# Performance work log

Measured on AMD Instinct MI355X. Metric: run time of the kernel, lower is better.

## Reference

```python
import jax, jax.numpy as jnp
import numpy as np

C = 256
NH = 4  # attention heads
G = 8   # groupnorm groups
EPS = 1e-5


def group_norm(x, weight, bias):
    B, Cc, H, W = x.shape
    xg = x.reshape(B, G, Cc // G, H, W)
    mean = xg.mean(axis=(2, 3, 4), keepdims=True)
    var = xg.var(axis=(2, 3, 4), keepdims=True)
    xg = (xg - mean) * jax.lax.rsqrt(var + EPS)
    xn = xg.reshape(B, Cc, H, W)
    return xn * weight[None, :, None, None] + bias[None, :, None, None]


def setup_inputs() -> dict:
    key = jax.random.key(0)
    ks = jax.random.split(key, 7)
    B, H, W = 16, 32, 32
    x = jax.random.normal(ks[0], (B, C, H, W), dtype=jnp.float32)
    n_weight = jnp.ones((C,), dtype=jnp.float32)
    n_bias = jnp.zeros((C,), dtype=jnp.float32)
    qkv_w = jax.random.normal(ks[1], (3 * C, C), dtype=jnp.float32) * (C ** -0.5)
    qkv_b = jnp.zeros((3 * C,), dtype=jnp.float32)
    p_w = jax.random.normal(ks[2], (C, C), dtype=jnp.float32) * (C ** -0.5)
    p_b = jnp.zeros((C,), dtype=jnp.float32)
    return {"x": x, "n_weight": n_weight, "n_bias": n_bias,
            "qkv_w": qkv_w, "qkv_b": qkv_b, "p_w": p_w, "p_b": p_b}


def reference(x, n_weight, n_bias, qkv_w, qkv_b, p_w, p_b):
    B, Cc, H, W = x.shape
    N = H * W
    dh = Cc // NH
    sc = dh ** -0.5
    xn = group_norm(x, n_weight, n_bias)  # [B,C,H,W]
    xn_flat = xn.reshape(B, Cc, N)
    # 1x1 conv == channel matmul
    qkv = jnp.einsum('oc,bcn->bon', qkv_w, xn_flat) + qkv_b[None, :, None]
    qkv = qkv.reshape(B, 3, NH, dh, N)
    q, k, v = qkv[:, 0], qkv[:, 1], qkv[:, 2]  # [B,h,dh,N]
    a = jax.nn.softmax(jnp.einsum('bhci,bhcj->bhij', q, k) * sc, axis=-1)
    o = jnp.einsum('bhij,bhcj->bhci', a, v).reshape(B, Cc, N)
    proj = jnp.einsum('oc,bcn->bon', p_w, o) + p_b[None, :, None]
    return x + proj.reshape(B, Cc, H, W)
```

## Files before the change

kernel.cpp:

```cpp
#include <hip/hip_runtime.h>
#include <math.h>

typedef unsigned short ushort;
typedef unsigned int uint;
typedef __attribute__((ext_vector_type(8))) short bf16x8;
typedef __attribute__((ext_vector_type(4))) float f32x4;

constexpr int Bc  = 16;
constexpr float EPSc = 1e-5f;
constexpr float QSC  = 0.18033688f;

__device__ inline ushort f2bf(float f) {
    uint u = __float_as_uint(f);
    uint r = (u + 0x7fffu + ((u >> 16) & 1u)) >> 16;
    return (ushort)r;
}
__device__ inline uint pack2(float a, float b) {
    return (uint)f2bf(a) | ((uint)f2bf(b) << 16);
}
__device__ __forceinline__ uint cvt2(float a, float b) {
#if __has_builtin(__builtin_amdgcn_cvt_pk_bf16_f32)
    auto v = __builtin_amdgcn_cvt_pk_bf16_f32(a, b);
    uint u; __builtin_memcpy(&u, &v, 4); return u;
#else
    return pack2(a, b);
#endif
}
#if __has_builtin(__builtin_amdgcn_exp2f)
#define EXP2F(x) __builtin_amdgcn_exp2f(x)
#else
#define EXP2F(x) __expf((x) * 0.69314718f)
#endif
__device__ __forceinline__ void gl_lds16(const ushort* g, ushort* l) {
    __builtin_amdgcn_global_load_lds(
        (const __attribute__((address_space(1))) void*)g,
        (__attribute__((address_space(3))) void*)l, 16, 0, 0);
}

__global__ __launch_bounds__(256) void pre_k(
    const float* __restrict__ x, const float* __restrict__ qkvw,
    const float* __restrict__ pw, float* __restrict__ pstats,
    ushort* __restrict__ wqb, ushort* __restrict__ pwb) {
    int blk = blockIdx.x;
    if (blk < 512) {
        int bg = blk >> 2, part = blk & 3;
        const float4* p = (const float4*)(x + (size_t)bg * 32768 + part * 8192);
        float s = 0.f, s2 = 0.f;
        for (int i = threadIdx.x; i < 2048; i += 256) {
            float4 v = p[i];
            s += v.x + v.y + v.z + v.w;
            s2 += v.x*v.x + v.y*v.y + v.z*v.z + v.w*v.w;
        }
        __shared__ float rs[256], rq[256];
        rs[threadIdx.x] = s; rq[threadIdx.x] = s2;
        __syncthreads();
        for (int off = 128; off > 0; off >>= 1) {
            if (threadIdx.x < (unsigned)off) {
                rs[threadIdx.x] += rs[threadIdx.x + off];
                rq[threadIdx.x] += rq[threadIdx.x + off];
            }
            __syncthreads();
        }
        if (threadIdx.x == 0) {
            pstats[blk * 2]     = rs[0];
            pstats[blk * 2 + 1] = rq[0];
        }
    } else {
        int idx = ((blk - 512) * 256 + threadIdx.x) * 4;
        if (idx < 196608) {
            int row = idx >> 8;
            float sc = (row < 256) ? QSC : 1.f;
            float4 v = *(const float4*)&qkvw[idx];
            uint2 u; u.x = pack2(v.x * sc, v.y * sc); u.y = pack2(v.z * sc, v.w * sc);
            *(uint2*)&wqb[idx] = u;
        } else {
            int j = idx - 196608;
            float4 v = *(const float4*)&pw[j];
            uint2 u; u.x = pack2(v.x, v.y); u.y = pack2(v.z, v.w);
            *(uint2*)&pwb[j] = u;
        }
    }
}

__global__ __launch_bounds__(256) void norm_t_k(
    const float* __restrict__ x, const float* __restrict__ pstats,
    const float* __restrict__ nw, const float* __restrict__ nb,
    ushort* __restrict__ xt) {
    int b = blockIdx.z, ct = blockIdx.y, nt = blockIdx.x;
    __shared__ ushort T[64 * 72];
    int t = threadIdx.x;
    int nn4 = (t & 15) * 4;
#pragma unroll
    for (int p = 0; p < 4; ++p) {
        int cl = (t >> 4) + p * 16;
        int c = ct * 64 + cl;
        int g = c >> 5;
        int base = (b * 8 + g) * 8;
        float s  = (pstats[base] + pstats[base+2]) + (pstats[base+4] + pstats[base+6]);
        float s2 = (pstats[base+1] + pstats[base+3]) + (pstats[base+5] + pstats[base+7]);
        float inv_n = 1.f / 32768.f;
        float mean = s * inv_n;
        float var  = s2 * inv_n - mean * mean;
        float inv  = rsqrtf(var + EPSc);
        float sw = inv * nw[c];
        float sb = nb[c] - mean * sw;
        float4 v = *(const float4*)&x[((size_t)(b * 256 + c)) * 1024 + nt * 64 + nn4];
        T[(nn4 + 0) * 72 + cl] = f2bf(v.x * sw + sb);
        T[(nn4 + 1) * 72 + cl] = f2bf(v.y * sw + sb);
        T[(nn4 + 2) * 72 + cl] = f2bf(v.z * sw + sb);
        T[(nn4 + 3) * 72 + cl] = f2bf(v.w * sw + sb);
    }
    __syncthreads();
#pragma unroll
    for (int p = 0; p < 4; ++p) {
        int nn = (t >> 4) + p * 16;
        int c4 = (t & 15) * 4;
        uint2 w = *(const uint2*)&T[nn * 72 + c4];
        *(uint2*)&xt[((size_t)b * 1024 + nt * 64 + nn) * 256 + ct * 64 + c4] = w;
    }
}

__global__ __launch_bounds__(256, 2) void qkv_gemm_k(
    const ushort* __restrict__ wq, const ushort* __restrict__ xt,
    const float* __restrict__ wb, ushort* __restrict__ qkT,
    ushort* __restrict__ vbuf) {
    int b = blockIdx.z, cy = blockIdx.y, sx = blockIdx.x;
    __shared__ ushort SB[2][2][128 * 64];
    int t = threadIdx.x, lane = t & 63, w = t >> 6;
    int quad = lane >> 4, l15 = lane & 15;
    int wm = w >> 1, wn = w & 1;
    const ushort* wrow = wq + (size_t)cy * 128 * 256;
    const ushort* xrow = xt + ((size_t)b * 1024 + sx * 128) * 256;
    bool tpath = (cy < 4);
    int r0 = t >> 3;
    int cs = (t & 7) ^ (r0 & 7);
    int dst = t * 8;
#pragma unroll
    for (int ps = 0; ps < 4; ++ps) {
        int r = r0 + ps * 32;
        gl_lds16(&wrow[(size_t)r * 256 + cs * 8], &SB[0][0][ps * 2048 + dst]);
        gl_lds16(&xrow[(size_t)r * 256 + cs * 8], &SB[0][1][ps * 2048 + dst]);
    }
    __syncthreads();
    int s0 = quad ^ (l15 & 7);
    f32x4 acc[4][4] = {};
    int cur = 0;
    for (int ki = 0; ki < 4; ++ki) {
        if (ki < 3) {
            int k0 = (ki + 1) * 64, nx = cur ^ 1;
#pragma unroll
            for (int ps = 0; ps < 4; ++ps) {
                int r = r0 + ps * 32;
                gl_lds16(&wrow[(size_t)r * 256 + k0 + cs * 8], &SB[nx][0][ps * 2048 + dst]);
                gl_lds16(&xrow[(size_t)r * 256 + k0 + cs * 8], &SB[nx][1][ps * 2048 + dst]);
            }
        }
        const ushort* Wc = SB[cur][0];
        const ushort* Xc = SB[cur][1];
        const ushort* Am = tpath ? Xc : Wc;
        const ushort* Bn = tpath ? Wc : Xc;
#pragma unroll
        for (int kk = 0; kk < 2; ++kk) {
            int sl = s0 ^ (kk * 4);
            bf16x8 fa[4], fb[4];
#pragma unroll
            for (int mi = 0; mi < 4; ++mi)
                fa[mi] = *(const bf16x8*)&Am[(wm * 64 + mi * 16 + l15) * 64 + sl * 8];
#pragma unroll
            for (int ni = 0; ni < 4; ++ni)
                fb[ni] = *(const bf16x8*)&Bn[(wn * 64 + ni * 16 + l15) * 64 + sl * 8];
#pragma unroll
            for (int mi = 0; mi < 4; ++mi)
#pragma unroll
                for (int ni = 0; ni < 4; ++ni)
                    acc[mi][ni] = __builtin_amdgcn_mfma_f32_16x16x32_bf16(
                        fa[mi], fb[ni], acc[mi][ni], 0, 0, 0);
        }
        __syncthreads();
        cur ^= 1;
    }
    ushort* Tw = ((ushort*)SB) + w * (64 * 72);
    float bsc = (tpath && cy < 2) ? QSC : 1.f;
    if (tpath) {
#pragma unroll
        for (int ni = 0; ni < 4; ++ni) {
            float bias = wb[cy * 128 + wn * 64 + ni * 16 + l15] * bsc;
#pragma unroll
            for (int mi = 0; mi < 4; ++mi)
#pragma unroll
                for (int rr = 0; rr < 4; ++rr)
                    Tw[(mi * 16 + quad * 4 + rr) * 72 + ni * 16 + l15] =
                        f2bf(acc[mi][ni][rr] + bias);
        }
    } else {
#pragma unroll
        for (int mi = 0; mi < 4; ++mi)
#pragma unroll
            for (int rr = 0; rr < 4; ++rr) {
                float bias = wb[cy * 128 + wm * 64 + mi * 16 + quad * 4 + rr];
#pragma unroll
                for (int ni = 0; ni < 4; ++ni)
                    Tw[(mi * 16 + quad * 4 + rr) * 72 + ni * 16 + l15] =
                        f2bf(acc[mi][ni][rr] + bias);
            }
    }
    __asm__ __volatile__("" ::: "memory");
    int row8 = lane >> 3, ch = lane & 7;
#pragma unroll
    for (int p = 0; p < 8; ++p) {
        int row = p * 8 + row8;
        uint4 u = *(const uint4*)&Tw[row * 72 + ch * 8];
        if (tpath) {
            int sp = sx * 128 + wm * 64 + row;
            *(uint4*)&qkT[((size_t)b * 1024 + sp) * 512 + cy * 128 + wn * 64 + ch * 8] = u;
        } else {
            int chanloc = (cy - 4) * 128 + wm * 64 + row;
            *(uint4*)&vbuf[((size_t)b * 256 + chanloc) * 1024 + sx * 128 + wn * 64 + ch * 8] = u;
        }
    }
}

__global__ __launch_bounds__(256, 3) void attn_k(
    const ushort* __restrict__ qkT, const ushort* __restrict__ vbuf,
    ushort* __restrict__ ot) {
    int i0 = blockIdx.x * 128;
    int bh = blockIdx.y;
    int b = bh >> 2, h = bh & 3;
    const ushort* qTb = qkT + (size_t)b * 1024 * 512 + h * 64;
    const ushort* kTb = qTb + 256;
    const ushort* vb  = vbuf + ((size_t)(b * 256 + h * 64)) * 1024;
    __shared__ ushort Ks[2][4096], Vs[2][4096];
    __shared__ ushort Ps[8 * 1152];
    __shared__ float  Lx[128];
    int t = threadIdx.x, lane = t & 63, w = t >> 6;
    int quad = lane >> 4, l15 = lane & 15;
    bf16x8 aq[2][2];
#pragma unroll
    for (int rb = 0; rb < 2; ++rb) {
        const ushort* qr = &qTb[(size_t)(i0 + rb * 64 + w * 16 + l15) * 512];
        aq[rb][0] = *(const bf16x8*)&qr[quad * 8];
        aq[rb][1] = *(const bf16x8*)&qr[32 + quad * 8];
    }
    int r0 = t >> 3;
    int cs = (t & 7) ^ (r0 & 7);
    int p0 = quad ^ (l15 & 7);
    int p1 = p0 ^ 4;
    gl_lds16(&kTb[(size_t)r0 * 512 + cs * 8],        &Ks[0][t * 8]);
    gl_lds16(&kTb[(size_t)(r0 + 32) * 512 + cs * 8], &Ks[0][t * 8 + 2048]);
    gl_lds16(&vb[(size_t)r0 * 1024 + cs * 8],        &Vs[0][t * 8]);
    gl_lds16(&vb[(size_t)(r0 + 32) * 1024 + cs * 8], &Vs[0][t * 8 + 2048]);
    __syncthreads();
    float lsum0 = 0.f, lsum1 = 0.f;
    f32x4 oacc[2][4] = {};
    ushort* Pw0 = &Ps[(w * 2 + 0) * 1152];
    ushort* Pw1 = &Ps[(w * 2 + 1) * 1152];
    int cur = 0;
    for (int j0 = 0; j0 < 1024; j0 += 64) {
        if (j0 < 960) {
            int jn = j0 + 64, nx = cur ^ 1;
            gl_lds16(&kTb[(size_t)(jn + r0) * 512 + cs * 8],        &Ks[nx][t * 8]);
            gl_lds16(&kTb[(size_t)(jn + r0 + 32) * 512 + cs * 8],   &Ks[nx][t * 8 + 2048]);
            gl_lds16(&vb[(size_t)r0 * 1024 + jn + cs * 8],          &Vs[nx][t * 8]);
            gl_lds16(&vb[(size_t)(r0 + 32) * 1024 + jn + cs * 8],   &Vs[nx][t * 8 + 2048]);
        }
        const ushort* Kc = Ks[cur];
        const ushort* Vc = Vs[cur];
        f32x4 s0[4], s1[4];
#pragma unroll
        for (int jt = 0; jt < 4; ++jt) {
            int row = jt * 16 + l15;
            bf16x8 bk0 = *(const bf16x8*)&Kc[row * 64 + p0 * 8];
            bf16x8 bk1 = *(const bf16x8*)&Kc[row * 64 + p1 * 8];
            f32x4 a = {0.f, 0.f, 0.f, 0.f};
            a = __builtin_amdgcn_mfma_f32_16x16x32_bf16(bk0, aq[0][0], a, 0, 0, 0);
            a = __builtin_amdgcn_mfma_f32_16x16x32_bf16(bk1, aq[0][1], a, 0, 0, 0);
            s0[jt] = a;
            f32x4 c = {0.f, 0.f, 0.f, 0.f};
            c = __builtin_amdgcn_mfma_f32_16x16x32_bf16(bk0, aq[1][0], c, 0, 0, 0);
            c = __builtin_amdgcn_mfma_f32_16x16x32_bf16(bk1, aq[1][1], c, 0, 0, 0);
            s1[jt] = c;
        }
#pragma unroll
        for (int jt = 0; jt < 4; ++jt) {
            int o = l15 * 72 + jt * 16 + quad * 4;
            float e0 = EXP2F(s0[jt][0]), e1 = EXP2F(s0[jt][1]);
            float e2 = EXP2F(s0[jt][2]), e3 = EXP2F(s0[jt][3]);
            lsum0 += (e0 + e1) + (e2 + e3);
            *(uint*)&Pw0[o]     = cvt2(e0, e1);
            *(uint*)&Pw0[o + 2] = cvt2(e2, e3);
            float f0 = EXP2F(s1[jt][0]), f1 = EXP2F(s1[jt][1]);
            float f2 = EXP2F(s1[jt][2]), f3 = EXP2F(s1[jt][3]);
            lsum1 += (f0 + f1) + (f2 + f3);
            *(uint*)&Pw1[o]     = cvt2(f0, f1);
            *(uint*)&Pw1[o + 2] = cvt2(f2, f3);
        }
        __asm__ __volatile__("" ::: "memory");
        bf16x8 ap00 = *(const bf16x8*)&Pw0[l15 * 72 + quad * 8];
        bf16x8 ap01 = *(const bf16x8*)&Pw0[l15 * 72 + 32 + quad * 8];
        bf16x8 ap10 = *(const bf16x8*)&Pw1[l15 * 72 + quad * 8];
        bf16x8 ap11 = *(const bf16x8*)&Pw1[l15 * 72 + 32 + quad * 8];
#pragma unroll
        for (int ct = 0; ct < 4; ++ct) {
            int row = ct * 16 + l15;
            bf16x8 bv0 = *(const bf16x8*)&Vc[row * 64 + p0 * 8];
            bf16x8 bv1 = *(const bf16x8*)&Vc[row * 64 + p1 * 8];
            oacc[0][ct] = __builtin_amdgcn_mfma_f32_16x16x32_bf16(ap00, bv0, oacc[0][ct], 0, 0, 0);
            oacc[0][ct] = __builtin_amdgcn_mfma_f32_16x16x32_bf16(ap01, bv1, oacc[0][ct], 0, 0, 0);
            oacc[1][ct] = __builtin_amdgcn_mfma_f32_16x16x32_bf16(ap10, bv0, oacc[1][ct], 0, 0, 0);
            oacc[1][ct] = __builtin_amdgcn_mfma_f32_16x16x32_bf16(ap11, bv1, oacc[1][ct], 0, 0, 0);
        }
        __syncthreads();
        cur ^= 1;
    }
    lsum0 += __shfl_xor(lsum0, 16); lsum0 += __shfl_xor(lsum0, 32);
    lsum1 += __shfl_xor(lsum1, 16); lsum1 += __shfl_xor(lsum1, 32);
    if (quad == 0) {
        Lx[w * 16 + l15]      = lsum0;
        Lx[64 + w * 16 + l15] = lsum1;
    }
    __asm__ __volatile__("" ::: "memory");
#pragma unroll
    for (int rb = 0; rb < 2; ++rb) {
        float4 lv = *(const float4*)&Lx[rb * 64 + w * 16 + quad * 4];
        float linv[4] = {1.f / lv.x, 1.f / lv.y, 1.f / lv.z, 1.f / lv.w};
        ushort* Pw = (rb == 0) ? Pw0 : Pw1;
#pragma unroll
        for (int ct = 0; ct < 4; ++ct)
#pragma unroll
            for (int rr = 0; rr < 4; ++rr)
                Pw[(quad * 4 + rr) * 72 + ct * 16 + l15] = f2bf(oacc[rb][ct][rr] * linv[rr]);
        __asm__ __volatile__("" ::: "memory");
#pragma unroll
        for (int p = 0; p < 2; ++p) {
            int row = p * 8 + (lane >> 3), ch = lane & 7;
            uint4 u = *(const uint4*)&Pw[row * 72 + ch * 8];
            *(uint4*)&ot[((size_t)b * 1024 + i0 + rb * 64 + w * 16 + row) * 256 + h * 64 + ch * 8] = u;
        }
    }
}

__global__ __launch_bounds__(256, 2) void proj_k(
    const ushort* __restrict__ pwb, const ushort* __restrict__ ot,
    const float* __restrict__ pb, const float* __restrict__ x,
    float* __restrict__ out) {
    int b = blockIdx.z, cy = blockIdx.y, sx = blockIdx.x;
    __shared__ ushort SB[2][2][128 * 64];
    int t = threadIdx.x, lane = t & 63, w = t >> 6;
    int quad = lane >> 4, l15 = lane & 15;
    int wm = w >> 1, wn = w & 1;
    const ushort* wrow = pwb + (size_t)cy * 128 * 256;
    const ushort* xrow = ot + ((size_t)b * 1024 + sx * 128) * 256;
    int r0 = t >> 3;
    int cs = (t & 7) ^ (r0 & 7);
    int dst = t * 8;
#pragma unroll
    for (int ps = 0; ps < 4; ++ps) {
        int r = r0 + ps * 32;
        gl_lds16(&wrow[(size_t)r * 256 + cs * 8], &SB[0][0][ps * 2048 + dst]);
        gl_lds16(&xrow[(size_t)r * 256 + cs * 8], &SB[0][1][ps * 2048 + dst]);
    }
    __syncthreads();
    int s0 = quad ^ (l15 & 7);
    f32x4 acc[4][4] = {};
    int cur = 0;
    for (int ki = 0; ki < 4; ++ki) {
        if (ki < 3) {
            int k0 = (ki + 1) * 64, nx = cur ^ 1;
#pragma unroll
            for (int ps = 0; ps < 4; ++ps) {
                int r = r0 + ps * 32;
                gl_lds16(&wrow[(size_t)r * 256 + k0 + cs * 8], &SB[nx][0][ps * 2048 + dst]);
                gl_lds16(&xrow[(size_t)r * 256 + k0 + cs * 8], &SB[nx][1][ps * 2048 + dst]);
            }
        }
        const ushort* Wc = SB[cur][0];
        const ushort* Xc = SB[cur][1];
#pragma unroll
        for (int kk = 0; kk < 2; ++kk) {
            int sl = s0 ^ (kk * 4);
            bf16x8 fa[4], fb[4];
#pragma unroll
            for (int mi = 0; mi < 4; ++mi)
                fa[mi] = *(const bf16x8*)&Wc[(wm * 64 + mi * 16 + l15) * 64 + sl * 8];
#pragma unroll
            for (int ni = 0; ni < 4; ++ni)
                fb[ni] = *(const bf16x8*)&Xc[(wn * 64 + ni * 16 + l15) * 64 + sl * 8];
#pragma unroll
            for (int mi = 0; mi < 4; ++mi)
#pragma unroll
                for (int ni = 0; ni < 4; ++ni)
                    acc[mi][ni] = __builtin_amdgcn_mfma_f32_16x16x32_bf16(
                        fa[mi], fb[ni], acc[mi][ni], 0, 0, 0);
        }
        __syncthreads();
        cur ^= 1;
    }
#pragma unroll
    for (int mi = 0; mi < 4; ++mi)
#pragma unroll
        for (int rr = 0; rr < 4; ++rr) {
            int chan = cy * 128 + wm * 64 + mi * 16 + quad * 4 + rr;
            float bias = pb[chan];
#pragma unroll
            for (int ni = 0; ni < 4; ++ni) {
                int sp = sx * 128 + wn * 64 + ni * 16 + l15;
                size_t o = ((size_t)(b * 256 + chan)) * 1024 + sp;
                out[o] = acc[mi][ni][rr] + bias + x[o];
            }
        }
}

extern "C" void kernel_launch(void* const* d_in, const int* in_sizes, int n_in,
                              void* d_out, int out_size, void* d_ws, size_t ws_size,
                              hipStream_t stream) {
    const float* x    = (const float*)d_in[0];
    const float* nw   = (const float*)d_in[1];
    const float* nb   = (const float*)d_in[2];
    const float* qkvw = (const float*)d_in[3];
    const float* qkvb = (const float*)d_in[4];
    const float* pw   = (const float*)d_in[5];
    const float* pb   = (const float*)d_in[6];
    float* out = (float*)d_out;

    float* pstats = (float*)d_ws;
    ushort* base = (ushort*)((char*)d_ws + 4096);
    ushort* xt   = base;
    ushort* wqb  = xt + (size_t)16 * 1024 * 256;
    ushort* pwb  = wqb + 768 * 256;
    ushort* qkT  = pwb + 256 * 256;
    ushort* vbuf = qkT + (size_t)16 * 1024 * 512;
    ushort* ot   = xt;

    pre_k<<<dim3(768), dim3(256), 0, stream>>>(x, qkvw, pw, pstats, wqb, pwb);
    norm_t_k<<<dim3(16, 4, Bc), dim3(256), 0, stream>>>(x, pstats, nw, nb, xt);
    qkv_gemm_k<<<dim3(8, 6, Bc), dim3(256), 0, stream>>>(wqb, xt, qkvb, qkT, vbuf);
    attn_k<<<dim3(8, 64), dim3(256), 0, stream>>>(qkT, vbuf, ot);
    proj_k<<<dim3(8, 2, Bc), dim3(256), 0, stream>>>(pwb, ot, pb, x, out);
}
```

Measured before the change: 138.0 us.

## Split attention keys across two blocks and merge partials in a combine kernel

The attention kernel now splits the 1024-key dimension into two halves along a new grid z axis, doubling the block count. Each half writes unnormalized bf16 partial outputs and per-row exp-sum partials, and a new combine kernel adds the halves and normalizes them. The projection GEMM switches to 64-wide spatial tiles so it launches twice as many blocks. A barrier is added before the QKV epilogue reuses shared memory. The aim is better CU occupancy, paid for with an extra launch, extra partial-buffer traffic and bf16 rounding of the unnormalized partials.

```diff
diff --git a/kernel.cpp b/kernel.cpp
--- a/kernel.cpp
+++ b/kernel.cpp
@@ -36,6 +36,8 @@
         (const __attribute__((address_space(1))) void*)g,
         (__attribute__((address_space(3))) void*)l, 16, 0, 0);
 }
+__device__ __forceinline__ float bfl(uint u) { return __uint_as_float(u << 16); }
+__device__ __forceinline__ float bfh(uint u) { return __uint_as_float(u & 0xffff0000u); }
 
 __global__ __launch_bounds__(256) void pre_k(
     const float* __restrict__ x, const float* __restrict__ qkvw,
@@ -179,6 +181,7 @@
         __syncthreads();
         cur ^= 1;
     }
+    __syncthreads();
     ushort* Tw = ((ushort*)SB) + w * (64 * 72);
     float bsc = (tpath && cy < 2) ? QSC : 1.f;
     if (tpath) {
@@ -222,16 +225,19 @@
 
 __global__ __launch_bounds__(256, 3) void attn_k(
     const ushort* __restrict__ qkT, const ushort* __restrict__ vbuf,
-    ushort* __restrict__ ot) {
+    ushort* __restrict__ op0, ushort* __restrict__ op1,
+    float* __restrict__ lpart) {
     int i0 = blockIdx.x * 128;
     int bh = blockIdx.y;
+    int jz = blockIdx.z;
     int b = bh >> 2, h = bh & 3;
     const ushort* qTb = qkT + (size_t)b * 1024 * 512 + h * 64;
-    const ushort* kTb = qTb + 256;
-    const ushort* vb  = vbuf + ((size_t)(b * 256 + h * 64)) * 1024;
+    const ushort* kTb = qTb + 256 + (size_t)jz * 512 * 512;
+    const ushort* vb  = vbuf + ((size_t)(b * 256 + h * 64)) * 1024 + jz * 512;
+    ushort* opart = jz ? op1 : op0;
+    float* lp = lpart + jz * 65536 + bh * 1024;
     __shared__ ushort Ks[2][4096], Vs[2][4096];
     __shared__ ushort Ps[8 * 1152];
-    __shared__ float  Lx[128];
     int t = threadIdx.x, lane = t & 63, w = t >> 6;
     int quad = lane >> 4, l15 = lane & 15;
     bf16x8 aq[2][2];
@@ -255,8 +261,8 @@
     ushort* Pw0 = &Ps[(w * 2 + 0) * 1152];
     ushort* Pw1 = &Ps[(w * 2 + 1) * 1152];
     int cur = 0;
-    for (int j0 = 0; j0 < 1024; j0 += 64) {
-        if (j0 < 960) {
+    for (int j0 = 0; j0 < 512; j0 += 64) {
+        if (j0 < 448) {
             int jn = j0 + 64, nx = cur ^ 1;
             gl_lds16(&kTb[(size_t)(jn + r0) * 512 + cs * 8],        &Ks[nx][t * 8]);
             gl_lds16(&kTb[(size_t)(jn + r0 + 32) * 512 + cs * 8],   &Ks[nx][t * 8 + 2048]);
@@ -315,80 +321,97 @@
     lsum0 += __shfl_xor(lsum0, 16); lsum0 += __shfl_xor(lsum0, 32);
     lsum1 += __shfl_xor(lsum1, 16); lsum1 += __shfl_xor(lsum1, 32);
     if (quad == 0) {
-        Lx[w * 16 + l15]      = lsum0;
-        Lx[64 + w * 16 + l15] = lsum1;
-    }
-    __asm__ __volatile__("" ::: "memory");
+        lp[i0 + w * 16 + l15]      = lsum0;
+        lp[i0 + 64 + w * 16 + l15] = lsum1;
+    }
 #pragma unroll
     for (int rb = 0; rb < 2; ++rb) {
-        float4 lv = *(const float4*)&Lx[rb * 64 + w * 16 + quad * 4];
-        float linv[4] = {1.f / lv.x, 1.f / lv.y, 1.f / lv.z, 1.f / lv.w};
         ushort* Pw = (rb == 0) ? Pw0 : Pw1;
 #pragma unroll
         for (int ct = 0; ct < 4; ++ct)
 #pragma unroll
             for (int rr = 0; rr < 4; ++rr)
-                Pw[(quad * 4 + rr) * 72 + ct * 16 + l15] = f2bf(oacc[rb][ct][rr] * linv[rr]);
+                Pw[(quad * 4 + rr) * 72 + ct * 16 + l15] = f2bf(oacc[rb][ct][rr]);
         __asm__ __volatile__("" ::: "memory");
 #pragma unroll
         for (int p = 0; p < 2; ++p) {
             int row = p * 8 + (lane >> 3), ch = lane & 7;
             uint4 u = *(const uint4*)&Pw[row * 72 + ch * 8];
-            *(uint4*)&ot[((size_t)b * 1024 + i0 + rb * 64 + w * 16 + row) * 256 + h * 64 + ch * 8] = u;
-        }
-    }
-}
-
-__global__ __launch_bounds__(256, 2) void proj_k(
+            *(uint4*)&opart[((size_t)b * 1024 + i0 + rb * 64 + w * 16 + row) * 256 + h * 64 + ch * 8] = u;
+        }
+    }
+}
+
+__global__ __launch_bounds__(256) void comb_k(
+    const ushort* __restrict__ op0, const ushort* __restrict__ op1,
+    const float* __restrict__ lpart, ushort* __restrict__ ot) {
+    int e8 = (blockIdx.x * 256 + threadIdx.x) * 8;
+    int b = e8 >> 18;
+    int i = (e8 >> 8) & 1023;
+    int c = e8 & 255;
+    int bh = b * 4 + (c >> 6);
+    float l = lpart[bh * 1024 + i] + lpart[65536 + bh * 1024 + i];
+    float linv = 1.f / l;
+    uint4 a = *(const uint4*)&op0[e8];
+    uint4 d = *(const uint4*)&op1[e8];
+    uint4 r;
+    r.x = cvt2((bfl(a.x) + bfl(d.x)) * linv, (bfh(a.x) + bfh(d.x)) * linv);
+    r.y = cvt2((bfl(a.y) + bfl(d.y)) * linv, (bfh(a.y) + bfh(d.y)) * linv);
+    r.z = cvt2((bfl(a.z) + bfl(d.z)) * linv, (bfh(a.z) + bfh(d.z)) * linv);
+    r.w = cvt2((bfl(a.w) + bfl(d.w)) * linv, (bfh(a.w) + bfh(d.w)) * linv);
+    *(uint4*)&ot[e8] = r;
+}
+
+__global__ __launch_bounds__(256, 3) void proj_k(
     const ushort* __restrict__ pwb, const ushort* __restrict__ ot,
     const float* __restrict__ pb, const float* __restrict__ x,
     float* __restrict__ out) {
     int b = blockIdx.z, cy = blockIdx.y, sx = blockIdx.x;
-    __shared__ ushort SB[2][2][128 * 64];
+    __shared__ ushort SB[2][12288];
     int t = threadIdx.x, lane = t & 63, w = t >> 6;
     int quad = lane >> 4, l15 = lane & 15;
     int wm = w >> 1, wn = w & 1;
     const ushort* wrow = pwb + (size_t)cy * 128 * 256;
-    const ushort* xrow = ot + ((size_t)b * 1024 + sx * 128) * 256;
+    const ushort* xrow = ot + ((size_t)b * 1024 + sx * 64) * 256;
     int r0 = t >> 3;
     int cs = (t & 7) ^ (r0 & 7);
     int dst = t * 8;
 #pragma unroll
-    for (int ps = 0; ps < 4; ++ps) {
-        int r = r0 + ps * 32;
-        gl_lds16(&wrow[(size_t)r * 256 + cs * 8], &SB[0][0][ps * 2048 + dst]);
-        gl_lds16(&xrow[(size_t)r * 256 + cs * 8], &SB[0][1][ps * 2048 + dst]);
-    }
+    for (int ps = 0; ps < 4; ++ps)
+        gl_lds16(&wrow[(size_t)(r0 + ps * 32) * 256 + cs * 8], &SB[0][ps * 2048 + dst]);
+#pragma unroll
+    for (int ps = 0; ps < 2; ++ps)
+        gl_lds16(&xrow[(size_t)(r0 + ps * 32) * 256 + cs * 8], &SB[0][8192 + ps * 2048 + dst]);
     __syncthreads();
-    int s0 = quad ^ (l15 & 7);
-    f32x4 acc[4][4] = {};
+    int p0 = quad ^ (l15 & 7);
+    f32x4 acc[4][2] = {};
     int cur = 0;
     for (int ki = 0; ki < 4; ++ki) {
         if (ki < 3) {
             int k0 = (ki + 1) * 64, nx = cur ^ 1;
 #pragma unroll
-            for (int ps = 0; ps < 4; ++ps) {
-                int r = r0 + ps * 32;
-                gl_lds16(&wrow[(size_t)r * 256 + k0 + cs * 8], &SB[nx][0][ps * 2048 + dst]);
-                gl_lds16(&xrow[(size_t)r * 256 + k0 + cs * 8], &SB[nx][1][ps * 2048 + dst]);
-            }
-        }
-        const ushort* Wc = SB[cur][0];
-        const ushort* Xc = SB[cur][1];
+            for (int ps = 0; ps < 4; ++ps)
+                gl_lds16(&wrow[(size_t)(r0 + ps * 32) * 256 + k0 + cs * 8], &SB[nx][ps * 2048 + dst]);
+#pragma unroll
+            for (int ps = 0; ps < 2; ++ps)
+                gl_lds16(&xrow[(size_t)(r0 + ps * 32) * 256 + k0 + cs * 8], &SB[nx][8192 + ps * 2048 + dst]);
+        }
+        const ushort* Wc = &SB[cur][0];
+        const ushort* Xc = &SB[cur][8192];
 #pragma unroll
         for (int kk = 0; kk < 2; ++kk) {
-            int sl = s0 ^ (kk * 4);
-            bf16x8 fa[4], fb[4];
+            int sl = p0 ^ (kk * 4);
+            bf16x8 fa[4], fb[2];
 #pragma unroll
             for (int mi = 0; mi < 4; ++mi)
                 fa[mi] = *(const bf16x8*)&Wc[(wm * 64 + mi * 16 + l15) * 64 + sl * 8];
 #pragma unroll
-            for (int ni = 0; ni < 4; ++ni)
-                fb[ni] = *(const bf16x8*)&Xc[(wn * 64 + ni * 16 + l15) * 64 + sl * 8];
+            for (int ni = 0; ni < 2; ++ni)
+                fb[ni] = *(const bf16x8*)&Xc[(wn * 32 + ni * 16 + l15) * 64 + sl * 8];
 #pragma unroll
             for (int mi = 0; mi < 4; ++mi)
 #pragma unroll
-                for (int ni = 0; ni < 4; ++ni)
+                for (int ni = 0; ni < 2; ++ni)
                     acc[mi][ni] = __builtin_amdgcn_mfma_f32_16x16x32_bf16(
                         fa[mi], fb[ni], acc[mi][ni], 0, 0, 0);
         }
@@ -402,8 +425,8 @@
             int chan = cy * 128 + wm * 64 + mi * 16 + quad * 4 + rr;
             float bias = pb[chan];
 #pragma unroll
-            for (int ni = 0; ni < 4; ++ni) {
-                int sp = sx * 128 + wn * 64 + ni * 16 + l15;
+            for (int ni = 0; ni < 2; ++ni) {
+                int sp = sx * 64 + wn * 32 + ni * 16 + l15;
                 size_t o = ((size_t)(b * 256 + chan)) * 1024 + sp;
                 out[o] = acc[mi][ni][rr] + bias + x[o];
             }
@@ -423,17 +446,21 @@
     float* out = (float*)d_out;
 
     float* pstats = (float*)d_ws;
-    ushort* base = (ushort*)((char*)d_ws + 4096);
+    float* lpart  = (float*)((char*)d_ws + 4096);
+    ushort* base = (ushort*)((char*)d_ws + 4096 + 524288);
     ushort* xt   = base;
     ushort* wqb  = xt + (size_t)16 * 1024 * 256;
     ushort* pwb  = wqb + 768 * 256;
     ushort* qkT  = pwb + 256 * 256;
     ushort* vbuf = qkT + (size_t)16 * 1024 * 512;
-    ushort* ot   = xt;
+    ushort* op0  = xt;
+    ushort* op1  = (ushort*)d_out;
+    ushort* ot   = vbuf;
 
     pre_k<<<dim3(768), dim3(256), 0, stream>>>(x, qkvw, pw, pstats, wqb, pwb);
     norm_t_k<<<dim3(16, 4, Bc), dim3(256), 0, stream>>>(x, pstats, nw, nb, xt);
     qkv_gemm_k<<<dim3(8, 6, Bc), dim3(256), 0, stream>>>(wqb, xt, qkvb, qkT, vbuf);
-    attn_k<<<dim3(8, 64), dim3(256), 0, stream>>>(qkT, vbuf, ot);
-    proj_k<<<dim3(8, 2, Bc), dim3(256), 0, stream>>>(pwb, ot, pb, x, out);
-}
+    attn_k<<<dim3(8, 64, 2), dim3(256), 0, stream>>>(qkT, vbuf, op0, op1, lpart);
+    comb_k<<<dim3(2048), dim3(256), 0, stream>>>(op0, op1, lpart, ot);
+    proj_k<<<dim3(16, 2, Bc), dim3(256), 0, stream>>>(pwb, ot, pb, x, out);
+}
```

After: 143.2 us. 3.8% more time.
